# Kernel tuning notes

Measured on AMD Instinct MI355X. Metric: run time of the kernel, lower is better.

Reference implementation:

```python
import jax, jax.numpy as jnp
import numpy as np

INF = 1e8
EPS = 1e-6
STRIDES = (8, 16, 32, 64, 128)
FEAT_SIZES = ((100, 128), (50, 64), (25, 32), (13, 16), (7, 8))
NUM_CLASSES = 81  # args.num_classes + 1
BG = NUM_CLASSES
TOPK1, TOPK2 = 3, 1
RATIO = 0.9
FRACTION = 0.5
B, G = 16, 32
NPER = [h * w for h, w in FEAT_SIZES]
OFFS = np.cumsum([0] + NPER)


def gen_trf():
    j = [2 ** i for i in range(8)]
    r1 = 1 + 6 * j[0]; r2 = r1 + 2 * j[1]
    p2 = r2 + 2 * j[2] * 3; r3 = p2 + 2 * j[2]
    p3 = r3 + 2 * j[3] * 3; r4 = p3 + 2 * j[3]
    p4 = r4 + 2 * j[4] * 5; r5 = p4 + 2 * j[4]
    p5 = r5 + 2 * j[5] * 2
    p6 = p5 + 2 * j[6]; p7 = p6 + 2 * j[7]
    return [p2, p3, p4, p5, p6, p7]


def make_points_rfields():
    trfs = gen_trf()
    pts, rfs = [], []
    for lvl, (h, w) in enumerate(FEAT_SIZES):
        s = STRIDES[lvl]
        xs = jnp.arange(w, dtype=jnp.float32) * s + s // 2
        ys = jnp.arange(h, dtype=jnp.float32) * s + s // 2
        Y, X = jnp.meshgrid(ys, xs, indexing='ij')
        p = jnp.stack([X.reshape(-1), Y.reshape(-1)], -1)
        pts.append(p)
        rf = trfs[lvl + 1] * FRACTION  # fpn_layer == 'p3' -> rfnum = lvl + 1
        rfs.append(jnp.concatenate([p - rf / 2, p + rf / 2], -1))
    return jnp.concatenate(pts, 0), jnp.concatenate(rfs, 0)


def kl_overlaps(gts, anc):
    # BboxDistanceMetric mode='kl': Gaussian KL divergence -> 1/(1+kl); (G, N)
    c1 = (gts[:, :2] + gts[:, 2:]) / 2
    c2 = (anc[:, :2] + anc[:, 2:]) / 2
    w1 = gts[:, 2] - gts[:, 0] + EPS; h1 = gts[:, 3] - gts[:, 1] + EPS
    w2 = anc[:, 2] - anc[:, 0] + EPS; h2 = anc[:, 3] - anc[:, 1] + EPS
    dx = c1[:, None, 0] - c2[None, :, 0]; dy = c1[:, None, 1] - c2[None, :, 1]
    w1s = (w1 ** 2)[:, None]; h1s = (h1 ** 2)[:, None]
    w2s = (w2 ** 2)[None, :]; h2s = (h2 ** 2)[None, :]
    kl = (w2s / w1s + h2s / h1s + 4 * dx ** 2 / w1s + 4 * dy ** 2 / h1s
          + jnp.log(w1s / w2s) + jnp.log(h1s / h2s) - 2) / 2
    return 1.0 / (1.0 + kl)


def hie_assign(rf1, rf2, gts):
    ov1 = kl_overlaps(gts, rf1)
    ov2 = kl_overlaps(gts, rf2)
    N = rf1.shape[0]; Gn = gts.shape[0]
    max_ov = ov1.max(0)
    assigned = jnp.where((max_ov >= 0) & (max_ov < 0.8), 0, -1).astype(jnp.int32)
    gt_ids = jnp.arange(1, Gn + 1, dtype=jnp.int32)
    _, i1 = jax.lax.top_k(ov1, TOPK1)  # (G, k1)
    s1 = jnp.full((N,), -1, jnp.int32).at[i1.reshape(-1)].max(jnp.repeat(gt_ids, TOPK1))
    assigned = jnp.where(s1 > 0, s1, assigned)
    _, i2 = jax.lax.top_k(ov2, TOPK2)  # (G, k2) second hierarchy overrides
    s2 = jnp.full((N,), -1, jnp.int32).at[i2.reshape(-1)].max(jnp.repeat(gt_ids, TOPK2))
    return jnp.where(s2 > 0, s2, assigned)


def target_single(gts, glabels, points, rf1, rf2):
    Gn = gts.shape[0]
    assigned = hie_assign(rf1, rf2, gts)  # (N,) 1-based gt index, 0/-1 = bg
    areas = (gts[:, 2] - gts[:, 0]) * (gts[:, 3] - gts[:, 1])
    mask = (assigned - 1)[:, None] == jnp.arange(Gn)[None, :]
    am = jnp.where(mask, areas[None, :], INF)
    min_area = am.min(1); mi = jnp.argmin(am, 1)
    lab = jnp.where(min_area >= INF, BG, glabels[mi])
    g = gts[mi]
    bt = jnp.stack([points[:, 0] - g[:, 0], points[:, 1] - g[:, 1],
                    g[:, 2] - points[:, 0], g[:, 3] - points[:, 1]], -1)
    return lab, bt


def diou_loss(pred, tgt):
    lt = jnp.maximum(pred[:, :2], tgt[:, :2])
    rb = jnp.minimum(pred[:, 2:], tgt[:, 2:])
    wh = jnp.clip(rb - lt, 0.0)
    ov = wh[:, 0] * wh[:, 1]
    ap = (pred[:, 2] - pred[:, 0]) * (pred[:, 3] - pred[:, 1])
    ag = (tgt[:, 2] - tgt[:, 0]) * (tgt[:, 3] - tgt[:, 1])
    ious = ov / (ap + ag - ov + EPS)
    elt = jnp.minimum(pred[:, :2], tgt[:, :2])
    erb = jnp.maximum(pred[:, 2:], tgt[:, 2:])
    ewh = jnp.clip(erb - elt, 0.0)
    c2 = ewh[:, 0] ** 2 + ewh[:, 1] ** 2 + EPS
    rho2 = ((pred[:, 0] + pred[:, 2] - tgt[:, 0] - tgt[:, 2]) ** 2
            + (pred[:, 1] + pred[:, 3] - tgt[:, 1] - tgt[:, 3]) ** 2) / 4
    return 1.0 - (ious - rho2 / c2)


def _forward(cls_l, bbox_l, ctr_l, gt_bboxes, gt_labels):
    points, rf1 = make_points_rfields()
    c = (rf1[:, :2] + rf1[:, 2:]) / 2
    wh = (rf1[:, 2:] - rf1[:, :2]) * RATIO
    rf2 = jnp.concatenate([c - wh / 2, c + wh / 2], -1)
    labels_all, targets_all = jax.vmap(target_single, (0, 0, None, None, None))(
        gt_bboxes, gt_labels, points, rf1, rf2)
    labels_all = jax.lax.stop_gradient(labels_all)
    targets_all = jax.lax.stop_gradient(targets_all)
    # flatten level-major, image-minor (matches torch.cat order in loss)
    fc = jnp.concatenate([t.transpose(0, 2, 3, 1).reshape(-1, NUM_CLASSES) for t in cls_l], 0)
    fb = jnp.concatenate([t.transpose(0, 2, 3, 1).reshape(-1, 4) for t in bbox_l], 0)
    fo = jnp.concatenate([t.transpose(0, 2, 3, 1).reshape(-1) for t in ctr_l], 0)
    fl = jnp.concatenate([labels_all[:, OFFS[i]:OFFS[i + 1]].reshape(-1) for i in range(5)], 0)
    ft = jnp.concatenate([targets_all[:, OFFS[i]:OFFS[i + 1]].reshape(-1, 4) for i in range(5)], 0)
    fp = jnp.concatenate([jnp.tile(points[OFFS[i]:OFFS[i + 1]], (B, 1)) for i in range(5)], 0)
    pos = fl < BG
    posf = pos.astype(fc.dtype)
    num_pos = jnp.maximum(posf.sum(), 1.0)
    # sigmoid focal loss (alpha=0.25, gamma=2); bg label -> all-zero one-hot
    tgt = jax.nn.one_hot(fl, NUM_CLASSES, dtype=fc.dtype)
    p = jax.nn.sigmoid(fc)
    pt = (1 - p) * tgt + p * (1 - tgt)
    fw = (0.25 * tgt + 0.75 * (1 - tgt)) * pt ** 2
    bce = jnp.maximum(fc, 0) - fc * tgt + jnp.log1p(jnp.exp(-jnp.abs(fc)))
    loss_cls = (bce * fw).sum() / num_pos
    # centerness target (sanitized on negatives to avoid nan)
    bt = jnp.where(pos[:, None], ft, 1.0)
    lr_min = jnp.minimum(bt[:, 0], bt[:, 2]); lr_max = jnp.maximum(bt[:, 0], bt[:, 2])
    tb_min = jnp.minimum(bt[:, 1], bt[:, 3]); tb_max = jnp.maximum(bt[:, 1], bt[:, 3])
    ctr_tgt = jnp.sqrt(jnp.clip((lr_min / lr_max) * (tb_min / tb_max), 0.0)) * posf
    denom = jnp.maximum(ctr_tgt.sum(), 1e-6)
    # decode distances to boxes and DIoU loss weighted by centerness
    x, y = fp[:, 0], fp[:, 1]
    pb = jnp.stack([x - fb[:, 0], y - fb[:, 1], x + fb[:, 2], y + fb[:, 3]], -1)
    tb_box = jnp.stack([x - bt[:, 0], y - bt[:, 1], x + bt[:, 2], y + bt[:, 3]], -1)
    loss_bbox = (diou_loss(pb, tb_box) * ctr_tgt).sum() / denom
    # centerness BCE-with-logits, averaged by num_pos
    bce_c = jnp.maximum(fo, 0) - fo * ctr_tgt + jnp.log1p(jnp.exp(-jnp.abs(fo)))
    loss_ctr = (bce_c * posf).sum() / num_pos
    return jnp.stack([loss_cls, loss_bbox, loss_ctr])


def setup_inputs() -> dict:
    key = jax.random.key(0)
    ks = jax.random.split(key, 24)
    cls_l = [jax.random.normal(ks[i], (B, NUM_CLASSES, h, w), jnp.float32) - 4.0
             for i, (h, w) in enumerate(FEAT_SIZES)]
    bbox_l = [jax.random.uniform(ks[5 + i], (B, 4, h, w), jnp.float32) * 64.0 + 1.0
              for i, (h, w) in enumerate(FEAT_SIZES)]
    ctr_l = [jax.random.normal(ks[10 + i], (B, 1, h, w), jnp.float32)
             for i, (h, w) in enumerate(FEAT_SIZES)]
    cx = jax.random.uniform(ks[15], (B, G)) * 1000.0 + 12.0
    cy = jax.random.uniform(ks[16], (B, G)) * 776.0 + 12.0
    w = jax.random.uniform(ks[17], (B, G)) * 240.0 + 8.0
    h = jax.random.uniform(ks[18], (B, G)) * 240.0 + 8.0
    gt_bboxes = jnp.stack([cx - w / 2, cy - h / 2, cx + w / 2, cy + h / 2], -1)
    gt_labels = jax.random.randint(ks[19], (B, G), 0, 80)
    d = {}
    for i in range(5):
        d[f'cls{i}'] = cls_l[i]; d[f'bbox{i}'] = bbox_l[i]; d[f'ctr{i}'] = ctr_l[i]
    d['gt_bboxes'] = gt_bboxes
    d['gt_labels'] = gt_labels
    return d


def reference(cls0, cls1, cls2, cls3, cls4, bbox0, bbox1, bbox2, bbox3, bbox4,
              ctr0, ctr1, ctr2, ctr3, ctr4, gt_bboxes, gt_labels):
    return _forward([cls0, cls1, cls2, cls3, cls4],
                    [bbox0, bbox1, bbox2, bbox3, bbox4],
                    [ctr0, ctr1, ctr2, ctr3, ctr4], gt_bboxes, gt_labels)
```

## Files before the change

### kernel.cpp

```cpp
#include <hip/hip_runtime.h>
#include <math.h>
#include <limits.h>

#pragma clang fp contract(off)

#define N_ANCH 17064
#define BATCH  16
#define NGT    32
#define BG_CLS 81
#define EPSF   1e-6f

#define NPB     512
#define NSTREAM 2048
#define L2E 1.44269504088896340736f
#define LN2 0.69314718055994530942f

#define C1   4147200
#define C2   5184000
#define C3   5443200
#define C4   5510592
#define TOT4 5528736

__device__ __forceinline__ float fexp2(float x){ return __builtin_amdgcn_exp2f(x); }
__device__ __forceinline__ float flog2(float x){ return __builtin_amdgcn_logf(x); }
__device__ __forceinline__ float frcp (float x){ return __builtin_amdgcn_rcpf(x); }

struct Geo { int lvl; int j; int HW; float px; float py; };

__device__ __forceinline__ Geo geom(int n) {
  Geo g;
  if (n < 12800)      { g.lvl=0; g.j=n;       g.HW=12800; g.px=(float)((g.j & 127)*8 + 4);   g.py=(float)((g.j >> 7)*8 + 4);   }
  else if (n < 16000) { g.lvl=1; g.j=n-12800; g.HW=3200;  g.px=(float)((g.j & 63)*16 + 8);   g.py=(float)((g.j >> 6)*16 + 8);  }
  else if (n < 16800) { g.lvl=2; g.j=n-16000; g.HW=800;   g.px=(float)((g.j & 31)*32 + 16);  g.py=(float)((g.j >> 5)*32 + 16); }
  else if (n < 17008) { g.lvl=3; g.j=n-16800; g.HW=208;   g.px=(float)((g.j & 15)*64 + 32);  g.py=(float)((g.j >> 4)*64 + 32); }
  else                { g.lvl=4; g.j=n-17008; g.HW=56;    g.px=(float)((g.j & 7)*128 + 64);  g.py=(float)((g.j >> 3)*128 + 64);}
  return g;
}

__device__ __forceinline__ bool bet(float av, int ai, float bv, int bi) {
  return (av < bv) || (av == bv && ai < bi);
}

__device__ __forceinline__ void insert3min(float* v, int* i, float nv, int ni) {
  if (nv < v[0])      { v[2]=v[1]; i[2]=i[1]; v[1]=v[0]; i[1]=i[0]; v[0]=nv; i[0]=ni; }
  else if (nv < v[1]) { v[2]=v[1]; i[2]=i[1]; v[1]=nv; i[1]=ni; }
  else                { v[2]=nv; i[2]=ni; }
}

__device__ __forceinline__ void insert3tie(float* v, int* i, float nv, int ni) {
  if (!bet(nv, ni, v[2], i[2])) return;
  if (bet(nv, ni, v[0], i[0]))      { v[2]=v[1]; i[2]=i[1]; v[1]=v[0]; i[1]=i[0]; v[0]=nv; i[0]=ni; }
  else if (bet(nv, ni, v[1], i[1])) { v[2]=v[1]; i[2]=i[1]; v[1]=nv; i[1]=ni; }
  else                              { v[2]=nv; i[2]=ni; }
}

__device__ __forceinline__ float negterm(float x) {
  float ax = fabsf(x);
  float e  = fexp2(ax * -L2E);
  float r  = frcp(1.0f + e);
  float p  = (x >= 0.0f) ? r : e * r;
  float sp = fmaxf(x, 0.0f) + flog2(1.0f + e) * LN2;
  return 0.75f * (p * p) * sp;
}

__global__ __launch_bounds__(256) void megaK(const float4* __restrict__ gtb,
                                             const float4* __restrict__ s0,
                                             const float4* __restrict__ s1,
                                             const float4* __restrict__ s2,
                                             const float4* __restrict__ s3,
                                             const float4* __restrict__ s4,
                                             int4* __restrict__ win,
                                             float* __restrict__ part,
                                             int* __restrict__ done) {
  __shared__ float sv[256 * 3];
  __shared__ int   si[256 * 3];
  __shared__ float tv[256];
  __shared__ int   ti[256];
  __shared__ float sh[256];

  int t = threadIdx.x;
  if (blockIdx.x == 0 && t == 0) *done = 0;

  if (blockIdx.x < NPB) {
    int blk = blockIdx.x;
    int b = blk >> 5, g = blk & 31;
    float4 GB = gtb[b * NGT + g];
    float c1x = (GB.x + GB.z) * 0.5f, c1y = (GB.y + GB.w) * 0.5f;
    float w1 = GB.z - GB.x + EPSF, h1 = GB.w - GB.y + EPSF;
    float w1s = w1 * w1, h1s = h1 * h1;
    float iw = 1.0f / w1s, ih = 1.0f / h1s;
    float iws = iw + ih;
    float Lg = logf(w1s) + logf(h1s);
    float Ay = 4.0f * ih;
    float Axc = 4.0f * iw;

    float v1[3] = {INFINITY, INFINITY, INFINITY};
    int   i1[3] = {INT_MAX, INT_MAX, INT_MAX};
    float v2 = INFINITY; int i2 = INT_MAX;

    #define DO_LEVEL(BASE, LGW, H, STRIDE, RF) do {                             \
      const int W_ = 1 << (LGW);                                                \
      float w2a = (RF) + 1e-6f;          float w2sa = w2a * w2a;                \
      float w2b = (RF) * 0.9f + 1e-6f;   float w2sb = w2b * w2b;                \
      float K1 = w2sa * iws + Lg - 2.0f * logf(w2sa) - 2.0f;                    \
      float K2 = w2sb * iws + Lg - 2.0f * logf(w2sb) - 2.0f;                    \
      int col = t & (W_ - 1);                                                   \
      float px = (float)(col * (STRIDE) + (STRIDE) / 2);                        \
      float dx = c1x - px;                                                      \
      float kx1 = Axc * dx * dx + K1;                                           \
      float kx2 = Axc * dx * dx + K2;                                           \
      int rstep = 256 >> (LGW);                                                 \
      for (int row = t >> (LGW); row < (H); row += rstep) {                     \
        float py = (float)(row * (STRIDE) + (STRIDE) / 2);                      \
        float dy = c1y - py;                                                    \
        float dy2 = dy * dy;                                                    \
        float k1 = fmaf(Ay, dy2, kx1);                                          \
        float k2 = fmaf(Ay, dy2, kx2);                                          \
        int n = (BASE) + (row << (LGW)) + col;                                  \
        if (k1 < v1[2]) insert3min(v1, i1, k1, n);                              \
        if (k2 < v2) { v2 = k2; i2 = n; }                                       \
      }                                                                         \
    } while (0)

    DO_LEVEL(0,     7, 100,   8,  45.5f);
    DO_LEVEL(12800, 6,  50,  16, 133.5f);
    DO_LEVEL(16000, 5,  25,  32, 213.5f);
    DO_LEVEL(16800, 4,  13,  64, 277.5f);
    DO_LEVEL(17008, 3,   7, 128, 405.5f);
    #undef DO_LEVEL

    sv[t*3+0] = v1[0]; sv[t*3+1] = v1[1]; sv[t*3+2] = v1[2];
    si[t*3+0] = i1[0]; si[t*3+1] = i1[1]; si[t*3+2] = i1[2];
    tv[t] = v2; ti[t] = i2;
    __syncthreads();
    for (int off = 128; off > 0; off >>= 1) {
      if (t < off) {
        #pragma unroll
        for (int k = 0; k < 3; ++k)
          insert3tie(&sv[t * 3], &si[t * 3], sv[(t + off) * 3 + k], si[(t + off) * 3 + k]);
        if (bet(tv[t + off], ti[t + off], tv[t], ti[t])) { tv[t] = tv[t + off]; ti[t] = ti[t + off]; }
      }
      __syncthreads();
    }
    if (t == 0) win[blk] = make_int4(si[0], si[1], si[2], ti[0]);
  } else {
    int sb = blockIdx.x - NPB;
    float local = 0.0f;
    for (int i = sb * 256 + t; i < TOT4; i += NSTREAM * 256) {
      const float4* p; int off;
      if (i < C1)      { p = s0; off = i; }
      else if (i < C2) { p = s1; off = i - C1; }
      else if (i < C3) { p = s2; off = i - C2; }
      else if (i < C4) { p = s3; off = i - C3; }
      else             { p = s4; off = i - C4; }
      float4 f = p[off];
      local += negterm(f.x);
      local += negterm(f.y);
      local += negterm(f.z);
      local += negterm(f.w);
    }
    sh[t] = local;
    __syncthreads();
    #pragma unroll
    for (int off = 128; off > 0; off >>= 1) {
      if (t < off) sh[t] += sh[t + off];
      __syncthreads();
    }
    if (t == 0) part[sb] = sh[0];
  }
}

__global__ __launch_bounds__(256) void resolveK(
    const int* __restrict__ win, const float4* __restrict__ gtb, const int* __restrict__ glab,
    const float* __restrict__ c0, const float* __restrict__ c1, const float* __restrict__ c2,
    const float* __restrict__ c3, const float* __restrict__ c4,
    const float* __restrict__ bb0, const float* __restrict__ bb1, const float* __restrict__ bb2,
    const float* __restrict__ bb3, const float* __restrict__ bb4,
    const float* __restrict__ ct0, const float* __restrict__ ct1, const float* __restrict__ ct2,
    const float* __restrict__ ct3, const float* __restrict__ ct4,
    const float* __restrict__ part,
    unsigned long long* __restrict__ bpart,
    int* __restrict__ done,
    float* __restrict__ out) {
  int t = threadIdx.x;
  int b = blockIdx.x;
  __shared__ unsigned int ukeys[128];

  if (t < 128) {
    int g = t >> 2, s = t & 3;
    int n = win[(b * NGT + g) * 4 + s];
    unsigned int pri = ((s == 3) ? 32u : 0u) + (unsigned int)g;
    ukeys[t] = (((unsigned int)n) << 6) | pri;
  }
  __syncthreads();

  double a_cls = 0.0, a_pos = 0.0, a_ctr = 0.0, a_diou = 0.0, a_cbce = 0.0;

  const float* clsA[5] = {c0, c1, c2, c3, c4};
  const float* bbA[5]  = {bb0, bb1, bb2, bb3, bb4};
  const float* ctA[5]  = {ct0, ct1, ct2, ct3, ct4};

  if (t < 128) {
    unsigned int me = ukeys[t];
    unsigned int nn = me >> 6;
    bool alive = true;
    #pragma unroll 8
    for (int j = 0; j < 128; ++j) {
      unsigned int o = ukeys[j];
      if ((o >> 6) == nn && o > me) alive = false;
    }
    if (alive) {
      int n = (int)nn;
      int g = (int)(me & 31u);
      int lab = glab[b * NGT + g];
      float4 gb = gtb[b * NGT + g];
      Geo G = geom(n);

      const float* bb = bbA[G.lvl];
      const float* ct = ctA[G.lvl];
      const float* cp = clsA[G.lvl];

      const float* bp = bb + b * 4 * G.HW + G.j;
      float f0 = bp[0];
      float f1 = bp[G.HW];
      float f2 = bp[2 * G.HW];
      float f3 = bp[3 * G.HW];
      float fo = ct[b * G.HW + G.j];
      float xc = cp[((size_t)(b * 81 + lab)) * G.HW + G.j];

      {
        float ax = fabsf(xc);
        float e  = fexp2(ax * -L2E);
        float r  = frcp(1.0f + e);
        float p  = (xc >= 0.0f) ? r : e * r;
        float sp = fmaxf(xc, 0.0f) + flog2(1.0f + e) * LN2;
        float neg = 0.75f * (p * p) * sp;
        float omp = 1.0f - p;
        float pos = 0.25f * (omp * omp) * (sp - xc);
        a_cls += (double)(pos - neg);
      }

      float tx = G.px - gb.x, ty = G.py - gb.y, tz = gb.z - G.px, tw = gb.w - G.py;

      float lr_min = fminf(tx, tz), lr_max = fmaxf(tx, tz);
      float tb_min = fminf(ty, tw), tb_max = fmaxf(ty, tw);
      float prod = (lr_min / lr_max) * (tb_min / tb_max);
      float ctrt = sqrtf(fmaxf(prod, 0.0f));

      float pb0 = G.px - f0, pb1 = G.py - f1, pb2 = G.px + f2, pb3 = G.py + f3;
      float tb0 = G.px - tx, tb1 = G.py - ty, tb2 = G.px + tz, tb3 = G.py + tw;

      float ltx = fmaxf(pb0, tb0), lty = fmaxf(pb1, tb1);
      float rbx = fminf(pb2, tb2), rby = fminf(pb3, tb3);
      float whx = fmaxf(rbx - ltx, 0.0f), why = fmaxf(rby - lty, 0.0f);
      float ovl = whx * why;
      float ap = (pb2 - pb0) * (pb3 - pb1);
      float ag = (tb2 - tb0) * (tb3 - tb1);
      float ious = ovl / (ap + ag - ovl + EPSF);
      float eltx = fminf(pb0, tb0), elty = fminf(pb1, tb1);
      float erbx = fmaxf(pb2, tb2), erby = fmaxf(pb3, tb3);
      float ewx = fmaxf(erbx - eltx, 0.0f), ewy = fmaxf(erby - elty, 0.0f);
      float c2v = ewx * ewx + ewy * ewy + EPSF;
      float sx = pb0 + pb2 - tb0 - tb2;
      float sy = pb1 + pb3 - tb1 - tb3;
      float rho2 = (sx * sx + sy * sy) * 0.25f;
      float dl = 1.0f - (ious - rho2 / c2v);

      a_pos  += 1.0;
      a_ctr  += (double)ctrt;
      a_diou += (double)(dl * ctrt);
      a_cbce += (double)(fmaxf(fo, 0.0f) - fo * ctrt + log1pf(expf(-fabsf(fo))));
    }
  }

  __shared__ double r0[256], r1[256], r2[256], r3[256], r4[256];
  r0[t] = a_cls; r1[t] = a_pos; r2[t] = a_ctr; r3[t] = a_diou; r4[t] = a_cbce;
  __syncthreads();
  #pragma unroll
  for (int off = 128; off > 0; off >>= 1) {
    if (t < off) {
      r0[t] += r0[t + off]; r1[t] += r1[t + off]; r2[t] += r2[t + off];
      r3[t] += r3[t + off]; r4[t] += r4[t + off];
    }
    __syncthreads();
  }

  __shared__ int lastFlag;
  if (t == 0) {
    atomicExch(&bpart[b * 5 + 0], __double_as_longlong(r0[0]));
    atomicExch(&bpart[b * 5 + 1], __double_as_longlong(r1[0]));
    atomicExch(&bpart[b * 5 + 2], __double_as_longlong(r2[0]));
    atomicExch(&bpart[b * 5 + 3], __double_as_longlong(r3[0]));
    atomicExch(&bpart[b * 5 + 4], __double_as_longlong(r4[0]));
    __threadfence();
    int old = atomicAdd(done, 1);
    lastFlag = (old == BATCH - 1) ? 1 : 0;
  }
  __syncthreads();
  if (!lastFlag) return;

  double c = 0.0;
  for (int i = t; i < NSTREAM; i += 256) c += (double)part[i];
  r0[t] = c;
  __syncthreads();
  #pragma unroll
  for (int off = 128; off > 0; off >>= 1) {
    if (t < off) r0[t] += r0[t + off];
    __syncthreads();
  }
  if (t == 0) {
    double sc = r0[0], sp = 0.0, sct = 0.0, sdi = 0.0, scb = 0.0;
    for (int i = 0; i < BATCH; ++i) {
      sc  += __longlong_as_double(atomicAdd(&bpart[i * 5 + 0], 0ull));
      sp  += __longlong_as_double(atomicAdd(&bpart[i * 5 + 1], 0ull));
      sct += __longlong_as_double(atomicAdd(&bpart[i * 5 + 2], 0ull));
      sdi += __longlong_as_double(atomicAdd(&bpart[i * 5 + 3], 0ull));
      scb += __longlong_as_double(atomicAdd(&bpart[i * 5 + 4], 0ull));
    }
    double np_ = sp > 1.0 ? sp : 1.0;
    double dn  = sct > 1e-6 ? sct : 1e-6;
    out[0] = (float)(sc / np_);
    out[1] = (float)(sdi / dn);
    out[2] = (float)(scb / np_);
  }
}

extern "C" void kernel_launch(void* const* d_in, const int* in_sizes, int n_in,
                              void* d_out, int out_size, void* d_ws, size_t ws_size,
                              hipStream_t stream) {
  (void)in_sizes; (void)n_in; (void)out_size; (void)ws_size;
  const float* cls[5] = {(const float*)d_in[0],  (const float*)d_in[3],  (const float*)d_in[6],
                         (const float*)d_in[9],  (const float*)d_in[12]};
  const float* bbx[5] = {(const float*)d_in[1],  (const float*)d_in[4],  (const float*)d_in[7],
                         (const float*)d_in[10], (const float*)d_in[13]};
  const float* ctr[5] = {(const float*)d_in[2],  (const float*)d_in[5],  (const float*)d_in[8],
                         (const float*)d_in[11], (const float*)d_in[14]};
  const float4* gtb = (const float4*)d_in[15];
  const int* glab = (const int*)d_in[16];

  char* ws = (char*)d_ws;
  int4*  win  = (int4*)ws;
  float* part = (float*)(ws + NPB * 16);
  int*   done = (int*)(ws + 16384);
  unsigned long long* bpart = (unsigned long long*)(ws + 16448);

  megaK<<<NPB + NSTREAM, 256, 0, stream>>>(gtb,
                                           (const float4*)cls[0], (const float4*)cls[1],
                                           (const float4*)cls[2], (const float4*)cls[3],
                                           (const float4*)cls[4],
                                           win, part, done);
  resolveK<<<BATCH, 256, 0, stream>>>((const int*)win, gtb, glab,
                                      cls[0], cls[1], cls[2], cls[3], cls[4],
                                      bbx[0], bbx[1], bbx[2], bbx[3], bbx[4],
                                      ctr[0], ctr[1], ctr[2], ctr[3], ctr[4],
                                      part, bpart, done, (float*)d_out);
}
```

Measured before the change: 45.85 us.

## Fuse assignment and resolve kernels with per-image last-block completion counters

Merges the two kernels into one launch. The last assignment block of each image does that image's resolve step, and a global counter picks one block to produce the final output. The streaming blocks now split their work per level by block range instead of branching on offset every iteration. Counters are zeroed with a memset and a launch-bounds occupancy hint is added. This removes the second kernel launch and its dependency gap, but adds a memset node, atomics and larger shared memory per block.

```diff
diff --git a/kernel.cpp b/kernel.cpp
--- a/kernel.cpp
+++ b/kernel.cpp
@@ -10,16 +10,10 @@
 #define BG_CLS 81
 #define EPSF   1e-6f
 
+#define NSTREAM 2048
 #define NPB     512
-#define NSTREAM 2048
 #define L2E 1.44269504088896340736f
 #define LN2 0.69314718055994530942f
-
-#define C1   4147200
-#define C2   5184000
-#define C3   5443200
-#define C4   5510592
-#define TOT4 5528736
 
 __device__ __forceinline__ float fexp2(float x){ return __builtin_amdgcn_exp2f(x); }
 __device__ __forceinline__ float flog2(float x){ return __builtin_amdgcn_logf(x); }
@@ -63,27 +57,102 @@
   return 0.75f * (p * p) * sp;
 }
 
-__global__ __launch_bounds__(256) void megaK(const float4* __restrict__ gtb,
-                                             const float4* __restrict__ s0,
-                                             const float4* __restrict__ s1,
-                                             const float4* __restrict__ s2,
-                                             const float4* __restrict__ s3,
-                                             const float4* __restrict__ s4,
-                                             int4* __restrict__ win,
-                                             float* __restrict__ part,
-                                             int* __restrict__ done) {
-  __shared__ float sv[256 * 3];
-  __shared__ int   si[256 * 3];
+__device__ __forceinline__ void final_combine(const float* __restrict__ part,
+                                              const double* __restrict__ bpart,
+                                              float* __restrict__ out,
+                                              double* r0s, int t) {
+  __threadfence();
+  double c = 0.0;
+  for (int i = t; i < NSTREAM; i += 256) c += (double)part[i];
+  r0s[t] = c;
+  __syncthreads();
+  #pragma unroll
+  for (int off = 128; off > 0; off >>= 1) {
+    if (t < off) r0s[t] += r0s[t + off];
+    __syncthreads();
+  }
+  if (t == 0) {
+    double sc = r0s[0], sp = 0.0, sct = 0.0, sdi = 0.0, scb = 0.0;
+    for (int i = 0; i < BATCH; ++i) {
+      sc  += bpart[i * 5 + 0];
+      sp  += bpart[i * 5 + 1];
+      sct += bpart[i * 5 + 2];
+      sdi += bpart[i * 5 + 3];
+      scb += bpart[i * 5 + 4];
+    }
+    double np_ = sp > 1.0 ? sp : 1.0;
+    double dn  = sct > 1e-6 ? sct : 1e-6;
+    out[0] = (float)(sc / np_);
+    out[1] = (float)(sdi / dn);
+    out[2] = (float)(scb / np_);
+  }
+}
+
+__global__ __launch_bounds__(256, 4) void fusedK(
+    const float4* __restrict__ gtb, const int* __restrict__ glab,
+    const float* __restrict__ c0, const float* __restrict__ c1, const float* __restrict__ c2,
+    const float* __restrict__ c3, const float* __restrict__ c4,
+    const float* __restrict__ bb0, const float* __restrict__ bb1, const float* __restrict__ bb2,
+    const float* __restrict__ bb3, const float* __restrict__ bb4,
+    const float* __restrict__ ct0, const float* __restrict__ ct1, const float* __restrict__ ct2,
+    const float* __restrict__ ct3, const float* __restrict__ ct4,
+    int* __restrict__ win, float* __restrict__ part, double* __restrict__ bpart,
+    int* __restrict__ done_img, int* __restrict__ done_sub, int* __restrict__ done_glb,
+    float* __restrict__ out) {
+  __shared__ float sv[768];
+  __shared__ int   si[768];
   __shared__ float tv[256];
   __shared__ int   ti[256];
   __shared__ float sh[256];
-
-  int t = threadIdx.x;
-  if (blockIdx.x == 0 && t == 0) *done = 0;
-
-  if (blockIdx.x < NPB) {
-    int blk = blockIdx.x;
-    int b = blk >> 5, g = blk & 31;
+  __shared__ unsigned int ukeys[128];
+  __shared__ double r0[256], r1[256], r2[256], r3[256], r4[256];
+  __shared__ int sflag;
+
+  int t  = threadIdx.x;
+  int bi = blockIdx.x;
+
+  if (bi < NSTREAM) {
+    const float4* p; int cnt, stride, sb;
+    if (bi < 1536)      { p = (const float4*)c0; cnt = 4147200; stride = 393216; sb = bi; }
+    else if (bi < 1920) { p = (const float4*)c1; cnt = 1036800; stride = 98304;  sb = bi - 1536; }
+    else if (bi < 2016) { p = (const float4*)c2; cnt = 259200;  stride = 24576;  sb = bi - 1920; }
+    else if (bi < 2041) { p = (const float4*)c3; cnt = 67392;   stride = 6400;   sb = bi - 2016; }
+    else                { p = (const float4*)c4; cnt = 18144;   stride = 1792;   sb = bi - 2041; }
+    float local = 0.0f;
+    for (int i = sb * 256 + t; i < cnt; i += stride) {
+      float4 f = p[i];
+      local += negterm(f.x);
+      local += negterm(f.y);
+      local += negterm(f.z);
+      local += negterm(f.w);
+    }
+    sh[t] = local;
+    __syncthreads();
+    #pragma unroll
+    for (int off = 128; off > 0; off >>= 1) {
+      if (t < off) sh[t] += sh[t + off];
+      __syncthreads();
+    }
+    if (t == 0) {
+      part[bi] = sh[0];
+      __threadfence();
+      int old = atomicAdd(&done_sub[bi & 15], 1);
+      int f = 0;
+      if (old == 127) {
+        __threadfence();
+        int old2 = atomicAdd(done_glb, 1);
+        f = (old2 == 31);
+      }
+      sflag = f;
+    }
+    __syncthreads();
+    if (sflag) final_combine(part, bpart, out, r0, t);
+    return;
+  }
+
+  int blk = bi - NSTREAM;
+  int b = blk >> 5, g = blk & 31;
+  {
     float4 GB = gtb[b * NGT + g];
     float c1x = (GB.x + GB.z) * 0.5f, c1y = (GB.y + GB.w) * 0.5f;
     float w1 = GB.z - GB.x + EPSF, h1 = GB.w - GB.y + EPSF;
@@ -142,63 +211,26 @@
       }
       __syncthreads();
     }
-    if (t == 0) win[blk] = make_int4(si[0], si[1], si[2], ti[0]);
-  } else {
-    int sb = blockIdx.x - NPB;
-    float local = 0.0f;
-    for (int i = sb * 256 + t; i < TOT4; i += NSTREAM * 256) {
-      const float4* p; int off;
-      if (i < C1)      { p = s0; off = i; }
-      else if (i < C2) { p = s1; off = i - C1; }
-      else if (i < C3) { p = s2; off = i - C2; }
-      else if (i < C4) { p = s3; off = i - C3; }
-      else             { p = s4; off = i - C4; }
-      float4 f = p[off];
-      local += negterm(f.x);
-      local += negterm(f.y);
-      local += negterm(f.z);
-      local += negterm(f.w);
-    }
-    sh[t] = local;
-    __syncthreads();
-    #pragma unroll
-    for (int off = 128; off > 0; off >>= 1) {
-      if (t < off) sh[t] += sh[t + off];
-      __syncthreads();
-    }
-    if (t == 0) part[sb] = sh[0];
-  }
-}
-
-__global__ __launch_bounds__(256) void resolveK(
-    const int* __restrict__ win, const float4* __restrict__ gtb, const int* __restrict__ glab,
-    const float* __restrict__ c0, const float* __restrict__ c1, const float* __restrict__ c2,
-    const float* __restrict__ c3, const float* __restrict__ c4,
-    const float* __restrict__ bb0, const float* __restrict__ bb1, const float* __restrict__ bb2,
-    const float* __restrict__ bb3, const float* __restrict__ bb4,
-    const float* __restrict__ ct0, const float* __restrict__ ct1, const float* __restrict__ ct2,
-    const float* __restrict__ ct3, const float* __restrict__ ct4,
-    const float* __restrict__ part,
-    unsigned long long* __restrict__ bpart,
-    int* __restrict__ done,
-    float* __restrict__ out) {
-  int t = threadIdx.x;
-  int b = blockIdx.x;
-  __shared__ unsigned int ukeys[128];
-
+    if (t == 0) {
+      ((int4*)win)[blk] = make_int4(si[0], si[1], si[2], ti[0]);
+      __threadfence();
+      int old = atomicAdd(&done_img[b], 1);
+      sflag = (old == 31);
+    }
+    __syncthreads();
+  }
+  if (!sflag) return;
+
+  __threadfence();
   if (t < 128) {
-    int g = t >> 2, s = t & 3;
-    int n = win[(b * NGT + g) * 4 + s];
-    unsigned int pri = ((s == 3) ? 32u : 0u) + (unsigned int)g;
+    int gg = t >> 2, s = t & 3;
+    int n = win[b * 128 + gg * 4 + s];
+    unsigned int pri = ((s == 3) ? 32u : 0u) + (unsigned int)gg;
     ukeys[t] = (((unsigned int)n) << 6) | pri;
   }
   __syncthreads();
 
   double a_cls = 0.0, a_pos = 0.0, a_ctr = 0.0, a_diou = 0.0, a_cbce = 0.0;
-
-  const float* clsA[5] = {c0, c1, c2, c3, c4};
-  const float* bbA[5]  = {bb0, bb1, bb2, bb3, bb4};
-  const float* ctA[5]  = {ct0, ct1, ct2, ct3, ct4};
 
   if (t < 128) {
     unsigned int me = ukeys[t];
@@ -211,14 +243,17 @@
     }
     if (alive) {
       int n = (int)nn;
-      int g = (int)(me & 31u);
-      int lab = glab[b * NGT + g];
-      float4 gb = gtb[b * NGT + g];
+      int gg = (int)(me & 31u);
+      int lab = glab[b * NGT + gg];
+      float4 gb = gtb[b * NGT + gg];
       Geo G = geom(n);
 
-      const float* bb = bbA[G.lvl];
-      const float* ct = ctA[G.lvl];
-      const float* cp = clsA[G.lvl];
+      const float* bb; const float* ct; const float* cp;
+      if (G.lvl == 0)      { bb = bb0; ct = ct0; cp = c0; }
+      else if (G.lvl == 1) { bb = bb1; ct = ct1; cp = c1; }
+      else if (G.lvl == 2) { bb = bb2; ct = ct2; cp = c2; }
+      else if (G.lvl == 3) { bb = bb3; ct = ct3; cp = c3; }
+      else                 { bb = bb4; ct = ct4; cp = c4; }
 
       const float* bp = bb + b * 4 * G.HW + G.j;
       float f0 = bp[0];
@@ -273,7 +308,6 @@
     }
   }
 
-  __shared__ double r0[256], r1[256], r2[256], r3[256], r4[256];
   r0[t] = a_cls; r1[t] = a_pos; r2[t] = a_ctr; r3[t] = a_diou; r4[t] = a_cbce;
   __syncthreads();
   #pragma unroll
@@ -285,44 +319,18 @@
     __syncthreads();
   }
 
-  __shared__ int lastFlag;
   if (t == 0) {
-    atomicExch(&bpart[b * 5 + 0], __double_as_longlong(r0[0]));
-    atomicExch(&bpart[b * 5 + 1], __double_as_longlong(r1[0]));
-    atomicExch(&bpart[b * 5 + 2], __double_as_longlong(r2[0]));
-    atomicExch(&bpart[b * 5 + 3], __double_as_longlong(r3[0]));
-    atomicExch(&bpart[b * 5 + 4], __double_as_longlong(r4[0]));
+    bpart[b * 5 + 0] = r0[0];
+    bpart[b * 5 + 1] = r1[0];
+    bpart[b * 5 + 2] = r2[0];
+    bpart[b * 5 + 3] = r3[0];
+    bpart[b * 5 + 4] = r4[0];
     __threadfence();
-    int old = atomicAdd(done, 1);
-    lastFlag = (old == BATCH - 1) ? 1 : 0;
+    int old2 = atomicAdd(done_glb, 1);
+    sflag = (old2 == 31);
   }
   __syncthreads();
-  if (!lastFlag) return;
-
-  double c = 0.0;
-  for (int i = t; i < NSTREAM; i += 256) c += (double)part[i];
-  r0[t] = c;
-  __syncthreads();
-  #pragma unroll
-  for (int off = 128; off > 0; off >>= 1) {
-    if (t < off) r0[t] += r0[t + off];
-    __syncthreads();
-  }
-  if (t == 0) {
-    double sc = r0[0], sp = 0.0, sct = 0.0, sdi = 0.0, scb = 0.0;
-    for (int i = 0; i < BATCH; ++i) {
-      sc  += __longlong_as_double(atomicAdd(&bpart[i * 5 + 0], 0ull));
-      sp  += __longlong_as_double(atomicAdd(&bpart[i * 5 + 1], 0ull));
-      sct += __longlong_as_double(atomicAdd(&bpart[i * 5 + 2], 0ull));
-      sdi += __longlong_as_double(atomicAdd(&bpart[i * 5 + 3], 0ull));
-      scb += __longlong_as_double(atomicAdd(&bpart[i * 5 + 4], 0ull));
-    }
-    double np_ = sp > 1.0 ? sp : 1.0;
-    double dn  = sct > 1e-6 ? sct : 1e-6;
-    out[0] = (float)(sc / np_);
-    out[1] = (float)(sdi / dn);
-    out[2] = (float)(scb / np_);
-  }
+  if (sflag) final_combine(part, bpart, out, r0, t);
 }
 
 extern "C" void kernel_launch(void* const* d_in, const int* in_sizes, int n_in,
@@ -339,19 +347,20 @@
   const int* glab = (const int*)d_in[16];
 
   char* ws = (char*)d_ws;
-  int4*  win  = (int4*)ws;
-  float* part = (float*)(ws + NPB * 16);
-  int*   done = (int*)(ws + 16384);
-  unsigned long long* bpart = (unsigned long long*)(ws + 16448);
-
-  megaK<<<NPB + NSTREAM, 256, 0, stream>>>(gtb,
-                                           (const float4*)cls[0], (const float4*)cls[1],
-                                           (const float4*)cls[2], (const float4*)cls[3],
-                                           (const float4*)cls[4],
-                                           win, part, done);
-  resolveK<<<BATCH, 256, 0, stream>>>((const int*)win, gtb, glab,
-                                      cls[0], cls[1], cls[2], cls[3], cls[4],
-                                      bbx[0], bbx[1], bbx[2], bbx[3], bbx[4],
-                                      ctr[0], ctr[1], ctr[2], ctr[3], ctr[4],
-                                      part, bpart, done, (float*)d_out);
-}
+  int*    win      = (int*)ws;
+  float*  part     = (float*)(ws + 8192);
+  double* bpart    = (double*)(ws + 16384);
+  int*    done_img = (int*)(ws + 17024);
+  int*    done_sub = (int*)(ws + 17088);
+  int*    done_glb = (int*)(ws + 17152);
+
+  hipMemsetAsync(ws + 17024, 0, 132, stream);
+
+  fusedK<<<NSTREAM + NPB, 256, 0, stream>>>(
+      gtb, glab,
+      cls[0], cls[1], cls[2], cls[3], cls[4],
+      bbx[0], bbx[1], bbx[2], bbx[3], bbx[4],
+      ctr[0], ctr[1], ctr[2], ctr[3], ctr[4],
+      win, part, bpart, done_img, done_sub, done_glb,
+      (float*)d_out);
+}
```

Measured after the change: 116.4 us. 2.54x slower.
